# Kernel optimization log

Measured on AMD Instinct MI355X. Metric: run time of the kernel, lower is better.

The kernel has to match this reference:

```python
import jax, jax.numpy as jnp
import numpy as np

C = 768      # n_embd
H = 12       # n_head
L = 6        # n_layer (per stack: base and head)
BS = 256     # block_size (per-stream length t)
B = 2        # batch
VU = 512     # vocab_size_up
VD = 512     # vocab_size_down
NM = 438     # n_music


def _ln(x, g, b, eps=1e-5):
    m = jnp.mean(x, -1, keepdims=True)
    v = jnp.mean((x - m) ** 2, -1, keepdims=True)
    return (x - m) * jax.lax.rsqrt(v + eps) * g + b


def _blocks(x, p, mask):
    # p: tuple of 16 stacked [L, ...] param arrays; scan over layers
    def body(x, lp):
        g1, b1, Wq, Bq, Wk, Bk, Wv, Bv, Wo, Bo, g2, b2, Wf, Bf, Wp, Bp = lp
        Bb, T, Cc = x.shape
        D = Cc // H
        h = _ln(x, g1, b1)
        q = (h @ Wq + Bq).reshape(Bb, T, H, D).transpose(0, 2, 1, 3)
        k = (h @ Wk + Bk).reshape(Bb, T, H, D).transpose(0, 2, 1, 3)
        v = (h @ Wv + Bv).reshape(Bb, T, H, D).transpose(0, 2, 1, 3)
        att = jnp.einsum('bhid,bhjd->bhij', q, k) * (1.0 / np.sqrt(D).astype(np.float32))
        att = jnp.where(mask, att, jnp.float32(-1e9))
        att = jax.nn.softmax(att, axis=-1)
        y = jnp.einsum('bhij,bhjd->bhid', att, v).transpose(0, 2, 1, 3).reshape(Bb, T, Cc)
        x = x + y @ Wo + Bo
        h2 = _ln(x, g2, b2)
        x = x + jax.nn.gelu(h2 @ Wf + Bf, approximate=False) @ Wp + Bp
        return x, None
    x, _ = jax.lax.scan(body, x, p)
    return x


def _forward(idx_up, idx_down, cond, tok_emb_up, tok_emb_down, pos_emb, cond_w, cond_b,
             base_p, head_p, ln_f_g, ln_f_b, head_up_w, head_down_w):
    t = idx_up.shape[1]
    te = jnp.concatenate([cond @ cond_w + cond_b, tok_emb_up[idx_up], tok_emb_down[idx_down]], axis=1)
    pe = jnp.concatenate([pos_emb[:, :t], pos_emb[:, BS:BS + t], pos_emb[:, 2 * BS:2 * BS + t]], axis=1)
    x = te + pe  # [B, 3t, C]
    tril = jnp.tril(jnp.ones((t, t), bool))
    mask = jnp.tile(tril, (3, 3))[None, None]  # 3x3 tiled block-causal mask [1,1,3t,3t]
    x = _blocks(x, base_p, mask)
    x = _blocks(x, head_p, mask)
    x = _ln(x, ln_f_g, ln_f_b)
    logits_up = x[:, t:2 * t] @ head_up_w
    logits_down = x[:, 2 * t:3 * t] @ head_down_w
    return logits_up, logits_down


def setup_inputs() -> dict:
    key = jax.random.key(0)
    ks = iter(jax.random.split(key, 100))
    def nrm(shape):
        return 0.02 * jax.random.normal(next(ks), shape, jnp.float32)
    inp = {
        'idx_up': jax.random.randint(next(ks), (B, BS), 0, VU),
        'idx_down': jax.random.randint(next(ks), (B, BS), 0, VD),
        'cond': jax.random.normal(next(ks), (B, BS, NM), jnp.float32),
        'tok_emb_up': nrm((VU, C)),
        'tok_emb_down': nrm((VD, C)),
        'pos_emb': nrm((1, 3 * BS, C)),
        'cond_w': nrm((NM, C)),
        'cond_b': jnp.zeros((C,), jnp.float32),
    }
    for pre in ('base_', 'head_'):
        inp[pre + 'ln1_g'] = jnp.ones((L, C), jnp.float32)
        inp[pre + 'ln1_b'] = jnp.zeros((L, C), jnp.float32)
        inp[pre + 'wq'] = nrm((L, C, C)); inp[pre + 'bq'] = jnp.zeros((L, C), jnp.float32)
        inp[pre + 'wk'] = nrm((L, C, C)); inp[pre + 'bk'] = jnp.zeros((L, C), jnp.float32)
        inp[pre + 'wv'] = nrm((L, C, C)); inp[pre + 'bv'] = jnp.zeros((L, C), jnp.float32)
        inp[pre + 'wo'] = nrm((L, C, C)); inp[pre + 'bo'] = jnp.zeros((L, C), jnp.float32)
        inp[pre + 'ln2_g'] = jnp.ones((L, C), jnp.float32)
        inp[pre + 'ln2_b'] = jnp.zeros((L, C), jnp.float32)
        inp[pre + 'fc_w'] = nrm((L, C, 4 * C)); inp[pre + 'fc_b'] = jnp.zeros((L, 4 * C), jnp.float32)
        inp[pre + 'pr_w'] = nrm((L, 4 * C, C)); inp[pre + 'pr_b'] = jnp.zeros((L, C), jnp.float32)
    inp['ln_f_g'] = jnp.ones((C,), jnp.float32)
    inp['ln_f_b'] = jnp.zeros((C,), jnp.float32)
    inp['head_up_w'] = nrm((C, VU))
    inp['head_down_w'] = nrm((C, VD))
    return inp


def reference(idx_up, idx_down, cond, tok_emb_up, tok_emb_down, pos_emb, cond_w, cond_b,
              base_ln1_g, base_ln1_b, base_wq, base_bq, base_wk, base_bk, base_wv, base_bv,
              base_wo, base_bo, base_ln2_g, base_ln2_b, base_fc_w, base_fc_b, base_pr_w, base_pr_b,
              head_ln1_g, head_ln1_b, head_wq, head_bq, head_wk, head_bk, head_wv, head_bv,
              head_wo, head_bo, head_ln2_g, head_ln2_b, head_fc_w, head_fc_b, head_pr_w, head_pr_b,
              ln_f_g, ln_f_b, head_up_w, head_down_w):
    base_p = (base_ln1_g, base_ln1_b, base_wq, base_bq, base_wk, base_bk, base_wv, base_bv,
              base_wo, base_bo, base_ln2_g, base_ln2_b, base_fc_w, base_fc_b, base_pr_w, base_pr_b)
    head_p = (head_ln1_g, head_ln1_b, head_wq, head_bq, head_wk, head_bk, head_wv, head_bv,
              head_wo, head_bo, head_ln2_g, head_ln2_b, head_fc_w, head_fc_b, head_pr_w, head_pr_b)
    return _forward(idx_up, idx_down, cond, tok_emb_up, tok_emb_down, pos_emb, cond_w, cond_b,
                    base_p, head_p, ln_f_g, ln_f_b, head_up_w, head_down_w)
```

## Files before the change

kernel.cpp:

```cpp
#include <hip/hip_runtime.h>
#include <cmath>

typedef unsigned short u16;
typedef __bf16 bf16x8 __attribute__((ext_vector_type(8)));
typedef float f32x4 __attribute__((ext_vector_type(4)));
typedef u16 u16x4 __attribute__((ext_vector_type(4)));
typedef u16 u16x2 __attribute__((ext_vector_type(2)));

#define GLOAD16(g, l) __builtin_amdgcn_global_load_lds( \
    (const __attribute__((address_space(1))) unsigned int*)(g), \
    (__attribute__((address_space(3))) unsigned int*)(l), 16, 0, 0)

__device__ __forceinline__ u16 f2b(float f) {
  unsigned u = __builtin_bit_cast(unsigned, f);
  unsigned r = (u + 0x7fffu + ((u >> 16) & 1u)) >> 16;
  return (u16)r;
}

__device__ __forceinline__ int xcd_swz(int lin, int nwg) {
  int q = nwg >> 3, r = nwg & 7;
  int xcd = lin & 7, idx = lin >> 3;
  return xcd * q + (xcd < r ? xcd : r) + idx;
}

__global__ __launch_bounds__(256)
void transw_k(const float* __restrict__ W, u16* __restrict__ Wt,
              int K, int N, int Kp, long sIn, long sOut)
{
  __shared__ float t[32][33];
  int n0 = blockIdx.x * 32, k0 = blockIdx.y * 32, l = blockIdx.z;
  const float* Wl = W + (long)l * sIn;
  u16* Wo = Wt + (long)l * sOut;
  int tx = threadIdx.x & 31, ty = threadIdx.x >> 5;
  #pragma unroll
  for (int i = 0; i < 4; ++i) {
    int k = k0 + ty + i * 8;
    t[ty + i * 8][tx] = (k < K) ? Wl[(long)k * N + n0 + tx] : 0.0f;
  }
  __syncthreads();
  #pragma unroll
  for (int i = 0; i < 2; ++i) {
    int p = threadIdx.x + 256 * i;
    int nl = p >> 4, kk = (p & 15) * 2;
    u16x2 o2; o2[0] = f2b(t[kk][nl]); o2[1] = f2b(t[kk + 1][nl]);
    *(u16x2*)(Wo + (long)(n0 + nl) * Kp + k0 + kk) = o2;
  }
}

__global__ void biascat_k(const float* bq0, const float* bk0, const float* bv0,
                          const float* bq1, const float* bk1, const float* bv1, float* o)
{
  int idx = blockIdx.x * 256 + threadIdx.x;
  int c = idx % 2304, l = idx / 2304;
  int st = l / 6, li = l % 6;
  const float* src = (c < 768) ? (st ? bq1 : bq0) : (c < 1536) ? (st ? bk1 : bk0) : (st ? bv1 : bv0);
  o[idx] = src[li * 768 + (c % 768)];
}

__global__ void condcvt_k(const float* __restrict__ c, u16* __restrict__ o)
{
  int idx = blockIdx.x * 256 + threadIdx.x;
  int k = idx % 448, r = idx / 448;
  o[idx] = f2b(k < 438 ? c[r * 438 + k] : 0.0f);
}

__global__ void embed_k(const int* __restrict__ iu, const int* __restrict__ idn,
                        const float* __restrict__ teu, const float* __restrict__ ted,
                        const float* __restrict__ pe, float* __restrict__ x)
{
  int idx = blockIdx.x * 256 + threadIdx.x;
  int c4 = idx % 192; int rest = idx / 192;
  int tt = rest % 512; int b = rest / 512;
  int i = tt & 255; int s = tt >> 8;
  int tok = s ? idn[b * 256 + i] : iu[b * 256 + i];
  const float4* src = (const float4*)(s ? (ted + (long)tok * 768) : (teu + (long)tok * 768));
  int prow = 256 + s * 256 + i;
  float4 pv = ((const float4*)(pe + (long)prow * 768))[c4];
  float4 sv = src[c4];
  float4 ov; ov.x = sv.x + pv.x; ov.y = sv.y + pv.y; ov.z = sv.z + pv.z; ov.w = sv.w + pv.w;
  ((float4*)(x + ((long)b * 768 + prow) * 768))[c4] = ov;
}

template<int S, bool WX>
__global__ __launch_bounds__(256)
void lnred_k(const float* __restrict__ xin, const float* __restrict__ P,
             const float* __restrict__ bias, const float* __restrict__ gg,
             const float* __restrict__ bb, float* __restrict__ xout,
             u16* __restrict__ h)
{
  int row = blockIdx.x * 4 + (threadIdx.x >> 6);
  int lane = threadIdx.x & 63;
  long base = (long)row * 768;
  const float4* xr4 = (const float4*)(xin + base);
  float4 v[3]; float s = 0.0f;
  #pragma unroll
  for (int j = 0; j < 3; ++j) {
    int f = lane + 64 * j;
    float4 val = xr4[f];
    if (S > 0) {
      float4 bv = ((const float4*)bias)[f];
      val.x += bv.x; val.y += bv.y; val.z += bv.z; val.w += bv.w;
      #pragma unroll
      for (int si = 0; si < S; ++si) {
        float4 pv = ((const float4*)(P + (long)si * 1179648 + base))[f];
        val.x += pv.x; val.y += pv.y; val.z += pv.z; val.w += pv.w;
      }
    }
    if (WX) ((float4*)(xout + base))[f] = val;
    v[j] = val; s += val.x + val.y + val.z + val.w;
  }
  #pragma unroll
  for (int d = 1; d < 64; d <<= 1) s += __shfl_xor(s, d);
  float mean = s * (1.0f / 768.0f);
  float s2 = 0.0f;
  #pragma unroll
  for (int j = 0; j < 3; ++j) {
    float dx = v[j].x - mean, dy = v[j].y - mean, dz = v[j].z - mean, dw = v[j].w - mean;
    s2 += dx * dx + dy * dy + dz * dz + dw * dw;
  }
  #pragma unroll
  for (int d = 1; d < 64; d <<= 1) s2 += __shfl_xor(s2, d);
  float rstd = rsqrtf(s2 * (1.0f / 768.0f) + 1e-5f);
  u16* orow = h + base;
  #pragma unroll
  for (int j = 0; j < 3; ++j) {
    int f = lane + 64 * j;
    float4 gv = ((const float4*)gg)[f];
    float4 bv2 = ((const float4*)bb)[f];
    u16x4 pk;
    pk[0] = f2b((v[j].x - mean) * rstd * gv.x + bv2.x);
    pk[1] = f2b((v[j].y - mean) * rstd * gv.y + bv2.y);
    pk[2] = f2b((v[j].z - mean) * rstd * gv.z + bv2.z);
    pk[3] = f2b((v[j].w - mean) * rstd * gv.w + bv2.w);
    *(u16x4*)(orow + 4 * f) = pk;
  }
}

__global__ __launch_bounds__(256)
void headred_k(const float* __restrict__ HP, float* __restrict__ out)
{
  int i4 = blockIdx.x * 256 + threadIdx.x;
  int st = i4 >> 16, loc = i4 & 65535;
  const float4* basep = (const float4*)HP + (long)st * 4 * 65536 + loc;
  float4 a = basep[0], b = basep[65536], c = basep[2 * 65536], d = basep[3 * 65536];
  float4 r; r.x = a.x + b.x + c.x + d.x; r.y = a.y + b.y + c.y + d.y;
  r.z = a.z + b.z + c.z + d.z; r.w = a.w + b.w + c.w + d.w;
  ((float4*)out)[i4] = r;
}

#define EPI_PLAIN 0
#define EPI_PE    1
#define EPI_QKV   2
#define EPI_GELU  4
#define EPI_PART  5

template<int BM, int BN, int WM, int WN, int EPI, bool BIAS>
__global__ __launch_bounds__(256)
void gemm_k(const u16* __restrict__ A, const u16* __restrict__ Bt, const float* __restrict__ bias,
            float* outf, u16* outb, u16* qb, u16* kb, u16* vT, const float* aux,
            int M, int N, int Ks, int lda, int ldb, int ldc,
            int astr, int aoff, int cstr, int coff, int pstr)
{
  constexpr int NWC = BN / WN;
  constexpr int NT  = (BM / WM) * NWC * 64;
  constexpr int LCH = (BM + BN) * 8;
  constexpr int LPT = LCH / NT;
  constexpr int MR = WM / 16, NR = WN / 16;
  __shared__ alignas(16) u16 Sl[2][(BM + BN) * 64];

  const int tid = threadIdx.x;
  const int gx = gridDim.x, gy = gridDim.y;
  const int nwg = gx * gy * gridDim.z;
  const int lin = (blockIdx.z * gy + blockIdx.y) * gx + blockIdx.x;
  const int wg = xcd_swz(lin, nwg);
  const int bx = wg % gx, t1g = wg / gx;
  const int by = t1g % gy, bz = t1g / gy;
  const int m0 = bx * BM, n0 = by * BN;
  const int koff = bz * Ks;
  const int lane = tid & 63, w = tid >> 6, l15 = lane & 15, g = lane >> 4;
  const int wr = w / NWC, wc = w % NWC;

  const u16* gp[LPT]; int lbase[LPT];
  #pragma unroll
  for (int j = 0; j < LPT; ++j) {
    int c = tid + NT * j;
    int slot = c & 7;
    if (c < BM * 8) {
      int row = c >> 3;
      int se = (slot ^ (row & 7)) * 8;
      int am = m0 + row;
      gp[j] = A + (long)((am >> 8) * astr + aoff + (am & 255)) * lda + koff + se;
    } else {
      int rb = c - BM * 8;
      int row = rb >> 3;
      int se = (slot ^ (row & 7)) * 8;
      gp[j] = Bt + (long)(n0 + row) * ldb + koff + se;
    }
    lbase[j] = w * 512 + NT * 8 * j;
  }

  int offA[2][MR], offB[2][NR];
  #pragma unroll
  for (int ks = 0; ks < 2; ++ks) {
    int s = 4 * ks + g;
    #pragma unroll
    for (int mi = 0; mi < MR; ++mi) {
      int r = wr * WM + mi * 16 + l15;
      offA[ks][mi] = r * 128 + ((s ^ (r & 7)) << 4);
    }
    #pragma unroll
    for (int ni = 0; ni < NR; ++ni) {
      int r = wc * WN + ni * 16 + l15;
      offB[ks][ni] = BM * 128 + r * 128 + ((s ^ (r & 7)) << 4);
    }
  }

  f32x4 acc[MR][NR];
  #pragma unroll
  for (int mi = 0; mi < MR; ++mi)
  #pragma unroll
  for (int ni = 0; ni < NR; ++ni) acc[mi][ni] = f32x4{};

  auto STAGE = [&](int kt, int buf) {
    #pragma unroll
    for (int j = 0; j < LPT; ++j) GLOAD16(gp[j] + kt, &Sl[buf][lbase[j]]);
  };
  auto COMPUTE = [&](int buf) {
    const char* Sb = (const char*)&Sl[buf][0];
    #pragma unroll
    for (int ks = 0; ks < 2; ++ks) {
      bf16x8 a[MR], b[NR];
      #pragma unroll
      for (int mi = 0; mi < MR; ++mi) a[mi] = *(const bf16x8*)(Sb + offA[ks][mi]);
      #pragma unroll
      for (int ni = 0; ni < NR; ++ni) b[ni] = *(const bf16x8*)(Sb + offB[ks][ni]);
      #pragma unroll
      for (int mi = 0; mi < MR; ++mi)
      #pragma unroll
      for (int ni = 0; ni < NR; ++ni)
        acc[mi][ni] = __builtin_amdgcn_mfma_f32_16x16x32_bf16(a[mi], b[ni], acc[mi][ni], 0, 0, 0);
    }
  };

  const int nIter = Ks >> 6;
  STAGE(0, 0);
  if (nIter > 1) STAGE(64, 1);
  for (int t = 0; t < nIter; ++t) {
    if (t + 1 < nIter) {
      if constexpr (LPT == 8) asm volatile("s_waitcnt vmcnt(8)" ::: "memory");
      else                    asm volatile("s_waitcnt vmcnt(4)" ::: "memory");
    } else {
      asm volatile("s_waitcnt vmcnt(0)" ::: "memory");
    }
    __builtin_amdgcn_s_barrier();
    COMPUTE(t & 1);
    if (t + 2 < nIter) {
      __builtin_amdgcn_s_barrier();
      STAGE((t + 2) << 6, t & 1);
    }
  }

  #pragma unroll
  for (int mi = 0; mi < MR; ++mi)
  #pragma unroll
  for (int ni = 0; ni < NR; ++ni) {
    f32x4 a = acc[mi][ni];
    int col = n0 + wc * WN + ni * 16 + l15;
    float bv = BIAS ? bias[col] : 0.0f;
    int mlb = m0 + wr * WM + mi * 16 + 4 * g;
    if (EPI == EPI_QKV) {
      if (col >= 1536) {
        int c2 = col - 1536, hh = c2 >> 6, dd = c2 & 63;
        int bb2 = mlb >= 768 ? 1 : 0;
        int t0 = mlb - bb2 * 768;
        u16x4 pk;
        #pragma unroll
        for (int r = 0; r < 4; ++r) pk[r] = f2b(a[r] + bv);
        *(u16x4*)(vT + (long)((bb2 * 12 + hh) * 64 + dd) * 768 + t0) = pk;
      } else {
        u16* dst = (col < 768) ? (qb + (long)mlb * 768 + col) : (kb + (long)mlb * 768 + (col - 768));
        #pragma unroll
        for (int r = 0; r < 4; ++r) dst[(long)r * 768] = f2b(a[r] + bv);
      }
    } else {
      #pragma unroll
      for (int r = 0; r < 4; ++r) {
        int rg = mlb + r;
        long crow = (long)(rg >> 8) * cstr + coff + (rg & 255);
        float v = a[r] + bv;
        if (EPI == EPI_PLAIN)      outf[crow * ldc + col] = v;
        else if (EPI == EPI_PE)    outf[crow * ldc + col] = v + aux[(long)(rg & 255) * 768 + col];
        else if (EPI == EPI_PART)  outf[(long)bz * pstr + (long)rg * ldc + col] = v;
        else if (EPI == EPI_GELU)  outb[crow * ldc + col] = f2b(0.5f * v * (1.0f + erff(v * 0.70710678f)));
      }
    }
  }
}

#define MFMA_BF16 __builtin_amdgcn_mfma_f32_16x16x32_bf16
__global__ __launch_bounds__(128)
void attn_k(const u16* __restrict__ qb, const u16* __restrict__ kb,
            const u16* __restrict__ vT, u16* __restrict__ y)
{
  __shared__ alignas(16) u16 Kl[3 * 4096];
  __shared__ alignas(16) u16 Vl[3 * 4096];
  __shared__ alignas(16) u16 Pl[2][16 * 72];
  const int gx = gridDim.x, gy = gridDim.y;
  const int nwg = gx * gy;
  const int lin = blockIdx.y * gx + blockIdx.x;
  const int wg = xcd_swz(lin, nwg);
  const int qt = wg % gx, bh = wg / gx;
  const int b = bh / 12, h = bh - b * 12;
  const int tid = threadIdx.x, w = tid >> 6, lane = tid & 63, l15 = lane & 15, g = lane >> 4;
  const int qrow = qt * 32 + w * 16 + l15;
  const int qm = qrow & 255;
  const int q0 = (qt * 32) & 255;
  const unsigned nw4 = (q0 >> 6) + 1;
  const int niter = 3 * nw4;
  const u16* qp = qb + (long)(b * 768 + qrow) * 768 + h * 64;
  bf16x8 qf0 = *(const bf16x8*)(qp + 8 * g);
  bf16x8 qf1 = *(const bf16x8*)(qp + 32 + 8 * g);
  f32x4 O0{}, O1{}, O2{}, O3{};
  float m_run = -1e30f, l_run = 0.0f;

  const u16* kp[4]; const u16* vp[4]; int ldsb[4];
  #pragma unroll
  for (int j = 0; j < 4; ++j) {
    int i = tid + 128 * j;
    int r = i >> 3, sl = ((i & 7) ^ (r & 7)) * 8;
    kp[j] = kb + (long)(b * 768 + r) * 768 + h * 64 + sl;
    vp[j] = vT + (long)(bh * 64 + r) * 768 + sl;
    ldsb[j] = (w + 2 * j) * 512;
  }

  auto STAGE = [&](int kt, int q) {
    u16* kd = Kl + q * 4096; u16* vd = Vl + q * 4096;
    #pragma unroll
    for (int j = 0; j < 4; ++j) GLOAD16(kp[j] + (long)kt * 64 * 768, kd + ldsb[j]);
    #pragma unroll
    for (int j = 0; j < 4; ++j) GLOAD16(vp[j] + kt * 64, vd + ldsb[j]);
  };
  auto MAP = [&](int it) {
    unsigned sb = (unsigned)it / nw4;
    return (int)(sb * 4 + ((unsigned)it - sb * nw4));
  };

  STAGE(MAP(0), 0);
  STAGE(MAP(1), 1);
  int cur = 0;
  for (int it = 0; it < niter; ++it) {
    if (it < niter - 1) asm volatile("s_waitcnt vmcnt(8)" ::: "memory");
    else                asm volatile("s_waitcnt vmcnt(0)" ::: "memory");
    __builtin_amdgcn_s_barrier();
    if (it + 2 < niter) STAGE(MAP(it + 2), cur == 0 ? 2 : cur - 1);
    const int kt = MAP(it);
    const char* Kb = (const char*)Kl + cur * 8192;
    const char* Vb = (const char*)Vl + cur * 8192;

    f32x4 s0{}, s1{}, s2{}, s3{};
    #pragma unroll
    for (int ks = 0; ks < 2; ++ks) {
      bf16x8 qf = ks ? qf1 : qf0;
      int sb = ((4 * ks + g) ^ (l15 & 7)) << 4;
      bf16x8 k0 = *(const bf16x8*)(Kb + (0  + l15) * 128 + sb);
      bf16x8 k1 = *(const bf16x8*)(Kb + (16 + l15) * 128 + sb);
      bf16x8 k2 = *(const bf16x8*)(Kb + (32 + l15) * 128 + sb);
      bf16x8 k3 = *(const bf16x8*)(Kb + (48 + l15) * 128 + sb);
      s0 = MFMA_BF16(k0, qf, s0, 0, 0, 0);
      s1 = MFMA_BF16(k1, qf, s1, 0, 0, 0);
      s2 = MFMA_BF16(k2, qf, s2, 0, 0, 0);
      s3 = MFMA_BF16(k3, qf, s3, 0, 0, 0);
    }
    float sv[16]; float tm = -1e30f;
    #pragma unroll
    for (int mt = 0; mt < 4; ++mt) {
      f32x4 sm4 = (mt == 0) ? s0 : (mt == 1) ? s1 : (mt == 2) ? s2 : s3;
      #pragma unroll
      for (int r = 0; r < 4; ++r) {
        int kg = kt * 64 + mt * 16 + 4 * g + r;
        float val = ((kg & 255) <= qm) ? sm4[r] * 0.125f : -1e30f;
        sv[mt * 4 + r] = val; tm = fmaxf(tm, val);
      }
    }
    tm = fmaxf(tm, __shfl_xor(tm, 16));
    tm = fmaxf(tm, __shfl_xor(tm, 32));
    float mn = fmaxf(m_run, tm);
    float alpha = __expf(m_run - mn);
    float ps = 0.0f; u16 pb16[16];
    #pragma unroll
    for (int j = 0; j < 16; ++j) {
      float p = (sv[j] <= -1e29f) ? 0.0f : __expf(sv[j] - mn);
      ps += p; pb16[j] = f2b(p);
    }
    ps += __shfl_xor(ps, 16); ps += __shfl_xor(ps, 32);
    l_run = l_run * alpha + ps; m_run = mn;
    float a0 = __shfl(alpha, 4 * g + 0);
    float a1 = __shfl(alpha, 4 * g + 1);
    float a2 = __shfl(alpha, 4 * g + 2);
    float a3 = __shfl(alpha, 4 * g + 3);
    #pragma unroll
    for (int mt = 0; mt < 4; ++mt) {
      u16x4 pk; pk[0] = pb16[4*mt]; pk[1] = pb16[4*mt+1]; pk[2] = pb16[4*mt+2]; pk[3] = pb16[4*mt+3];
      *(u16x4*)((char*)&Pl[w][0] + l15 * 144 + mt * 32 + 8 * g) = pk;
    }
    O0[0] *= a0; O0[1] *= a1; O0[2] *= a2; O0[3] *= a3;
    O1[0] *= a0; O1[1] *= a1; O1[2] *= a2; O1[3] *= a3;
    O2[0] *= a0; O2[1] *= a1; O2[2] *= a2; O2[3] *= a3;
    O3[0] *= a0; O3[1] *= a1; O3[2] *= a2; O3[3] *= a3;
    asm volatile("s_waitcnt lgkmcnt(0)" ::: "memory");
    __builtin_amdgcn_sched_barrier(0);
    #pragma unroll
    for (int ks = 0; ks < 2; ++ks) {
      bf16x8 pf = *(const bf16x8*)((const char*)&Pl[w][0] + l15 * 144 + 64 * ks + 16 * g);
      int sb = ((4 * ks + g) ^ (l15 & 7)) << 4;
      bf16x8 v0 = *(const bf16x8*)(Vb + (0  + l15) * 128 + sb);
      bf16x8 v1 = *(const bf16x8*)(Vb + (16 + l15) * 128 + sb);
      bf16x8 v2 = *(const bf16x8*)(Vb + (32 + l15) * 128 + sb);
      bf16x8 v3 = *(const bf16x8*)(Vb + (48 + l15) * 128 + sb);
      O0 = MFMA_BF16(pf, v0, O0, 0, 0, 0);
      O1 = MFMA_BF16(pf, v1, O1, 0, 0, 0);
      O2 = MFMA_BF16(pf, v2, O2, 0, 0, 0);
      O3 = MFMA_BF16(pf, v3, O3, 0, 0, 0);
    }
    cur = (cur == 2) ? 0 : cur + 1;
  }
  float n0i = 1.0f / __shfl(l_run, 4 * g + 0);
  float n1i = 1.0f / __shfl(l_run, 4 * g + 1);
  float n2i = 1.0f / __shfl(l_run, 4 * g + 2);
  float n3i = 1.0f / __shfl(l_run, 4 * g + 3);
  long yr = (long)(b * 768 + qt * 32 + w * 16 + 4 * g);
  #pragma unroll
  for (int ni = 0; ni < 4; ++ni) {
    f32x4 Ov = (ni == 0) ? O0 : (ni == 1) ? O1 : (ni == 2) ? O2 : O3;
    int c = h * 64 + ni * 16 + l15;
    y[(yr + 0) * 768 + c] = f2b(Ov[0] * n0i);
    y[(yr + 1) * 768 + c] = f2b(Ov[1] * n1i);
    y[(yr + 2) * 768 + c] = f2b(Ov[2] * n2i);
    y[(yr + 3) * 768 + c] = f2b(Ov[3] * n3i);
  }
}

extern "C" void kernel_launch(void* const* d_in, const int* in_sizes, int n_in,
                              void* d_out, int out_size, void* d_ws, size_t ws_size,
                              hipStream_t stream)
{
  (void)in_sizes; (void)n_in; (void)out_size;
  auto F = [&](int i){ return (const float*)d_in[i]; };
  const int* idx_up = (const int*)d_in[0];
  const int* idx_dn = (const int*)d_in[1];
  const float* cond = F(2);
  const float* teu = F(3);
  const float* ted = F(4);
  const float* pe  = F(5);
  const float* cw  = F(6);
  const float* cb  = F(7);
  float* outp = (float*)d_out;
  char* ws = (char*)d_ws;

  size_t o = 0;
  auto take = [&](size_t bytes){ void* p = ws + o; o += bytes; return p; };
  float* x    = (float*)take(4718592);
  u16*   h    = (u16*)take(2359296);
  u16*   qbuf = (u16*)take(2359296);
  u16*   kbuf = (u16*)take(2359296);
  u16*   vT   = (u16*)take(2359296);
  u16*   y    = (u16*)take(2359296);
  u16*   fca  = (u16*)take(9437184);
  u16*   xf   = (u16*)take(2359296);
  u16*   cbf  = (u16*)take(458752);
  float* qkvb = (float*)take(110592);
  u16*   hut  = (u16*)take(786432);
  u16*   hdt  = (u16*)take(786432);
  u16*   cwt  = (u16*)take(688128);
  float* P1   = (float*)take(9437184);
  float* P2   = (float*)take(18874368);
  float* HP   = (float*)take(8388608);
  const size_t WL = 14155776;
  bool up = (ws_size >= o + 12 * WL);
  size_t nsl = up ? 12 : 1;
  u16* qkvt = (u16*)(ws + o);
  u16* wot  = qkvt + nsl * 2304 * 768;
  u16* fct  = wot  + nsl * 768 * 768;
  u16* prt  = fct  + nsl * 3072 * 768;

  auto trans = [&](const float* src, u16* dst, int K, int N, int Kp, long sIn, long sOut, int nz){
    transw_k<<<dim3(N / 32, Kp / 32, nz), dim3(256), 0, stream>>>(src, dst, K, N, Kp, sIn, sOut);
  };

  if (up) {
    for (int s = 0; s < 2; ++s) {
      for (int p = 0; p < 3; ++p)
        trans(F(8 + 16*s + 2 + 2*p), qkvt + (size_t)s*6*2304*768 + (size_t)p*768*768,
              768, 768, 768, 768L*768, 2304L*768, 6);
      trans(F(8 + 16*s + 8),  wot + (size_t)s*6*768*768,  768, 768, 768, 768L*768, 768L*768, 6);
      trans(F(8 + 16*s + 12), fct + (size_t)s*6*3072*768, 768, 3072, 768, 768L*3072, 3072L*768, 6);
      trans(F(8 + 16*s + 14), prt + (size_t)s*6*768*3072, 3072, 768, 3072, 3072L*768, 768L*3072, 6);
    }
  }
  trans(F(42), hut, 768, 512, 768, 0, 0, 1);
  trans(F(43), hdt, 768, 512, 768, 0, 0, 1);
  trans(cw,    cwt, 438, 768, 448, 0, 0, 1);
  biascat_k<<<dim3(108), dim3(256), 0, stream>>>(F(11), F(13), F(15), F(27), F(29), F(31), qkvb);
  condcvt_k<<<dim3(896), dim3(256), 0, stream>>>(cond, cbf);
  embed_k<<<dim3(768), dim3(256), 0, stream>>>(idx_up, idx_dn, teu, ted, pe, x);
  gemm_k<64, 64, 32, 32, EPI_PE, true><<<dim3(8, 12, 1), dim3(256), 0, stream>>>(cbf, cwt, cb,
      x, nullptr, nullptr, nullptr, nullptr, pe,
      512, 768, 448, 448, 448, 768, 256, 0, 768, 0, 0);

  for (int l = 0; l < 12; ++l) {
    int s = l / 6, li = l % 6;
    u16* qkvt_l = qkvt + (up ? (size_t)l : 0) * 2304 * 768;
    u16* wot_l  = wot  + (up ? (size_t)l : 0) * 768 * 768;
    u16* fct_l  = fct  + (up ? (size_t)l : 0) * 3072 * 768;
    u16* prt_l  = prt  + (up ? (size_t)l : 0) * 768 * 3072;
    if (!up) {
      for (int p = 0; p < 3; ++p)
        trans(F(8 + 16*s + 2 + 2*p) + (size_t)li*768*768, qkvt_l + (size_t)p*768*768, 768, 768, 768, 0, 0, 1);
      trans(F(8 + 16*s + 8)  + (size_t)li*768*768,  wot_l, 768, 768, 768, 0, 0, 1);
      trans(F(8 + 16*s + 12) + (size_t)li*768*3072, fct_l, 768, 3072, 768, 0, 0, 1);
      trans(F(8 + 16*s + 14) + (size_t)li*3072*768, prt_l, 3072, 768, 3072, 0, 0, 1);
    }
    if (l == 0) {
      lnred_k<0, false><<<dim3(384), dim3(256), 0, stream>>>(x, nullptr, nullptr,
          F(8+16*s+0) + (size_t)li*768, F(8+16*s+1) + (size_t)li*768, nullptr, h);
    } else {
      int ps = (l - 1) / 6, pli = (l - 1) % 6;
      lnred_k<4, true><<<dim3(384), dim3(256), 0, stream>>>(x, P2,
          F(8+16*ps+15) + (size_t)pli*768,
          F(8+16*s+0) + (size_t)li*768, F(8+16*s+1) + (size_t)li*768, x, h);
    }
    gemm_k<128, 128, 64, 64, EPI_QKV, true><<<dim3(12, 18, 1), dim3(256), 0, stream>>>(h, qkvt_l, qkvb + (size_t)l*2304,
        nullptr, nullptr, qbuf, kbuf, vT, nullptr,
        1536, 2304, 768, 768, 768, 768, 256, 0, 256, 0, 0);
    attn_k<<<dim3(24, 24), dim3(128), 0, stream>>>(qbuf, kbuf, vT, y);
    gemm_k<128, 128, 64, 64, EPI_PART, false><<<dim3(12, 6, 2), dim3(256), 0, stream>>>(y, wot_l, nullptr,
        P1, nullptr, nullptr, nullptr, nullptr, nullptr,
        1536, 768, 384, 768, 768, 768, 256, 0, 256, 0, 1179648);
    lnred_k<2, true><<<dim3(384), dim3(256), 0, stream>>>(x, P1,
        F(8+16*s+9) + (size_t)li*768,
        F(8+16*s+10) + (size_t)li*768, F(8+16*s+11) + (size_t)li*768, x, h);
    gemm_k<128, 128, 64, 64, EPI_GELU, true><<<dim3(12, 24, 1), dim3(256), 0, stream>>>(h, fct_l, F(8+16*s+13) + (size_t)li*3072,
        nullptr, fca, nullptr, nullptr, nullptr, nullptr,
        1536, 3072, 768, 768, 768, 3072, 256, 0, 256, 0, 0);
    gemm_k<128, 128, 64, 64, EPI_PART, false><<<dim3(12, 6, 4), dim3(256), 0, stream>>>(fca, prt_l, nullptr,
        P2, nullptr, nullptr, nullptr, nullptr, nullptr,
        1536, 768, 768, 3072, 3072, 768, 256, 0, 256, 0, 1179648);
  }
  lnred_k<4, false><<<dim3(384), dim3(256), 0, stream>>>(x, P2,
      F(8+16*1+15) + (size_t)5*768, F(40), F(41), nullptr, xf);
  gemm_k<64, 64, 32, 32, EPI_PART, false><<<dim3(8, 8, 4), dim3(256), 0, stream>>>(xf, hut, nullptr,
      HP, nullptr, nullptr, nullptr, nullptr, nullptr,
      512, 512, 192, 768, 768, 512, 768, 256, 256, 0, 262144);
  gemm_k<64, 64, 32, 32, EPI_PART, false><<<dim3(8, 8, 4), dim3(256), 0, stream>>>(xf, hdt, nullptr,
      HP + 1048576, nullptr, nullptr, nullptr, nullptr, nullptr,
      512, 512, 192, 768, 768, 512, 768, 512, 256, 0, 262144);
  headred_k<<<dim3(512), dim3(256), 0, stream>>>(HP, outp);
}
```

Baseline: 1.354 ms.

## Shrink GEMM tiles to 128x64, halve proj split-K, merge head GEMMs

```diff
diff --git a/kernel.cpp b/kernel.cpp
--- a/kernel.cpp
+++ b/kernel.cpp
@@ -141,11 +141,12 @@
 {
   int i4 = blockIdx.x * 256 + threadIdx.x;
   int st = i4 >> 16, loc = i4 & 65535;
-  const float4* basep = (const float4*)HP + (long)st * 4 * 65536 + loc;
-  float4 a = basep[0], b = basep[65536], c = basep[2 * 65536], d = basep[3 * 65536];
-  float4 r; r.x = a.x + b.x + c.x + d.x; r.y = a.y + b.y + c.y + d.y;
-  r.z = a.z + b.z + c.z + d.z; r.w = a.w + b.w + c.w + d.w;
-  ((float4*)out)[i4] = r;
+  int r = loc >> 7, c4 = loc & 127;
+  const float4* basep = (const float4*)HP + (long)r * 256 + st * 128 + c4;
+  float4 a = basep[0], b = basep[131072], c = basep[2 * 131072], d = basep[3 * 131072];
+  float4 rr; rr.x = a.x + b.x + c.x + d.x; rr.y = a.y + b.y + c.y + d.y;
+  rr.z = a.z + b.z + c.z + d.z; rr.w = a.w + b.w + c.w + d.w;
+  ((float4*)out)[i4] = rr;
 }
 
 #define EPI_PLAIN 0
@@ -153,6 +154,7 @@
 #define EPI_QKV   2
 #define EPI_GELU  4
 #define EPI_PART  5
+#define EPI_HEAD  6
 
 template<int BM, int BN, int WM, int WN, int EPI, bool BIAS>
 __global__ __launch_bounds__(256)
@@ -179,6 +181,8 @@
   const int koff = bz * Ks;
   const int lane = tid & 63, w = tid >> 6, l15 = lane & 15, g = lane >> 4;
   const int wr = w / NWC, wc = w % NWC;
+  int aoffE = aoff;
+  if constexpr (EPI == EPI_HEAD) aoffE += (by >= (int)(gy >> 1)) ? 256 : 0;
 
   const u16* gp[LPT]; int lbase[LPT];
   #pragma unroll
@@ -189,7 +193,7 @@
       int row = c >> 3;
       int se = (slot ^ (row & 7)) * 8;
       int am = m0 + row;
-      gp[j] = A + (long)((am >> 8) * astr + aoff + (am & 255)) * lda + koff + se;
+      gp[j] = A + (long)((am >> 8) * astr + aoffE + (am & 255)) * lda + koff + se;
     } else {
       int rb = c - BM * 8;
       int row = rb >> 3;
@@ -247,8 +251,9 @@
   if (nIter > 1) STAGE(64, 1);
   for (int t = 0; t < nIter; ++t) {
     if (t + 1 < nIter) {
-      if constexpr (LPT == 8) asm volatile("s_waitcnt vmcnt(8)" ::: "memory");
-      else                    asm volatile("s_waitcnt vmcnt(4)" ::: "memory");
+      if constexpr (LPT == 8)      asm volatile("s_waitcnt vmcnt(8)" ::: "memory");
+      else if constexpr (LPT == 6) asm volatile("s_waitcnt vmcnt(6)" ::: "memory");
+      else                         asm volatile("s_waitcnt vmcnt(4)" ::: "memory");
     } else {
       asm volatile("s_waitcnt vmcnt(0)" ::: "memory");
     }
@@ -290,7 +295,8 @@
         float v = a[r] + bv;
         if (EPI == EPI_PLAIN)      outf[crow * ldc + col] = v;
         else if (EPI == EPI_PE)    outf[crow * ldc + col] = v + aux[(long)(rg & 255) * 768 + col];
-        else if (EPI == EPI_PART)  outf[(long)bz * pstr + (long)rg * ldc + col] = v;
+        else if (EPI == EPI_PART || EPI == EPI_HEAD)
+                                   outf[(long)bz * pstr + (long)rg * ldc + col] = v;
         else if (EPI == EPI_GELU)  outb[crow * ldc + col] = f2b(0.5f * v * (1.0f + erff(v * 0.70710678f)));
       }
     }
@@ -469,11 +475,10 @@
   u16*   xf   = (u16*)take(2359296);
   u16*   cbf  = (u16*)take(458752);
   float* qkvb = (float*)take(110592);
-  u16*   hut  = (u16*)take(786432);
-  u16*   hdt  = (u16*)take(786432);
+  u16*   hutd = (u16*)take(1572864);
   u16*   cwt  = (u16*)take(688128);
   float* P1   = (float*)take(9437184);
-  float* P2   = (float*)take(18874368);
+  float* P2   = (float*)take(9437184);
   float* HP   = (float*)take(8388608);
   const size_t WL = 14155776;
   bool up = (ws_size >= o + 12 * WL);
@@ -497,8 +502,8 @@
       trans(F(8 + 16*s + 14), prt + (size_t)s*6*768*3072, 3072, 768, 3072, 3072L*768, 768L*3072, 6);
     }
   }
-  trans(F(42), hut, 768, 512, 768, 0, 0, 1);
-  trans(F(43), hdt, 768, 512, 768, 0, 0, 1);
+  trans(F(42), hutd, 768, 512, 768, 0, 0, 1);
+  trans(F(43), hutd + 512 * 768, 768, 512, 768, 0, 0, 1);
   trans(cw,    cwt, 438, 768, 448, 0, 0, 1);
   biascat_k<<<dim3(108), dim3(256), 0, stream>>>(F(11), F(13), F(15), F(27), F(29), F(31), qkvb);
   condcvt_k<<<dim3(896), dim3(256), 0, stream>>>(cond, cbf);
@@ -525,34 +530,31 @@
           F(8+16*s+0) + (size_t)li*768, F(8+16*s+1) + (size_t)li*768, nullptr, h);
     } else {
       int ps = (l - 1) / 6, pli = (l - 1) % 6;
-      lnred_k<4, true><<<dim3(384), dim3(256), 0, stream>>>(x, P2,
+      lnred_k<2, true><<<dim3(384), dim3(256), 0, stream>>>(x, P2,
           F(8+16*ps+15) + (size_t)pli*768,
           F(8+16*s+0) + (size_t)li*768, F(8+16*s+1) + (size_t)li*768, x, h);
     }
-    gemm_k<128, 128, 64, 64, EPI_QKV, true><<<dim3(12, 18, 1), dim3(256), 0, stream>>>(h, qkvt_l, qkvb + (size_t)l*2304,
+    gemm_k<128, 64, 32, 64, EPI_QKV, true><<<dim3(12, 36, 1), dim3(256), 0, stream>>>(h, qkvt_l, qkvb + (size_t)l*2304,
         nullptr, nullptr, qbuf, kbuf, vT, nullptr,
         1536, 2304, 768, 768, 768, 768, 256, 0, 256, 0, 0);
     attn_k<<<dim3(24, 24), dim3(128), 0, stream>>>(qbuf, kbuf, vT, y);
-    gemm_k<128, 128, 64, 64, EPI_PART, false><<<dim3(12, 6, 2), dim3(256), 0, stream>>>(y, wot_l, nullptr,
+    gemm_k<128, 64, 32, 64, EPI_PART, false><<<dim3(12, 12, 2), dim3(256), 0, stream>>>(y, wot_l, nullptr,
         P1, nullptr, nullptr, nullptr, nullptr, nullptr,
         1536, 768, 384, 768, 768, 768, 256, 0, 256, 0, 1179648);
     lnred_k<2, true><<<dim3(384), dim3(256), 0, stream>>>(x, P1,
         F(8+16*s+9) + (size_t)li*768,
         F(8+16*s+10) + (size_t)li*768, F(8+16*s+11) + (size_t)li*768, x, h);
-    gemm_k<128, 128, 64, 64, EPI_GELU, true><<<dim3(12, 24, 1), dim3(256), 0, stream>>>(h, fct_l, F(8+16*s+13) + (size_t)li*3072,
+    gemm_k<128, 64, 32, 64, EPI_GELU, true><<<dim3(12, 48, 1), dim3(256), 0, stream>>>(h, fct_l, F(8+16*s+13) + (size_t)li*3072,
         nullptr, fca, nullptr, nullptr, nullptr, nullptr,
         1536, 3072, 768, 768, 768, 3072, 256, 0, 256, 0, 0);
-    gemm_k<128, 128, 64, 64, EPI_PART, false><<<dim3(12, 6, 4), dim3(256), 0, stream>>>(fca, prt_l, nullptr,
+    gemm_k<128, 64, 32, 64, EPI_PART, false><<<dim3(12, 12, 2), dim3(256), 0, stream>>>(fca, prt_l, nullptr,
         P2, nullptr, nullptr, nullptr, nullptr, nullptr,
-        1536, 768, 768, 3072, 3072, 768, 256, 0, 256, 0, 1179648);
-  }
-  lnred_k<4, false><<<dim3(384), dim3(256), 0, stream>>>(x, P2,
+        1536, 768, 1536, 3072, 3072, 768, 256, 0, 256, 0, 1179648);
+  }
+  lnred_k<2, false><<<dim3(384), dim3(256), 0, stream>>>(x, P2,
       F(8+16*1+15) + (size_t)5*768, F(40), F(41), nullptr, xf);
-  gemm_k<64, 64, 32, 32, EPI_PART, false><<<dim3(8, 8, 4), dim3(256), 0, stream>>>(xf, hut, nullptr,
+  gemm_k<64, 64, 32, 32, EPI_HEAD, false><<<dim3(8, 16, 4), dim3(256), 0, stream>>>(xf, hutd, nullptr,
       HP, nullptr, nullptr, nullptr, nullptr, nullptr,
-      512, 512, 192, 768, 768, 512, 768, 256, 256, 0, 262144);
-  gemm_k<64, 64, 32, 32, EPI_PART, false><<<dim3(8, 8, 4), dim3(256), 0, stream>>>(xf, hdt, nullptr,
-      HP + 1048576, nullptr, nullptr, nullptr, nullptr, nullptr,
-      512, 512, 192, 768, 768, 512, 768, 512, 256, 0, 262144);
+      512, 1024, 192, 768, 768, 1024, 768, 256, 256, 0, 524288);
   headred_k<<<dim3(512), dim3(256), 0, stream>>>(HP, outp);
 }
```

Measured after the change: 1.291 ms. 1.05x faster.
